# Optimization experiments

Measured on AMD Instinct MI355X. Metric: run time of the kernel, lower is better.

Reference implementation:

```python
import jax, jax.numpy as jnp
import numpy as np

B = 2_000_000
HID = 50
DIM = 2


def setup_inputs() -> dict:
    key = jax.random.key(0)
    k_y, k_w1, k_w2 = jax.random.split(key, 3)
    y = jax.random.normal(k_y, (B, DIM), dtype=jnp.float32)
    # weights ~ N(0, 0.1), biases = 0, matching the torch init
    W1 = 0.1 * jax.random.normal(k_w1, (HID, DIM), dtype=jnp.float32)
    b1 = jnp.zeros((HID,), dtype=jnp.float32)
    W2 = 0.1 * jax.random.normal(k_w2, (DIM, HID), dtype=jnp.float32)
    b2 = jnp.zeros((DIM,), dtype=jnp.float32)
    t = jnp.float32(0.0)
    return {"t": t, "y": y, "W1": W1, "b1": b1, "W2": W2, "b2": b2}


def reference(t, y, W1, b1, W2, b2):
    # Linear(2->50) + tanh + Linear(50->2); t is unused by the ODE func body.
    h = jnp.tanh(y @ W1.T + b1)  # [B, 50]
    return h @ W2.T + b2          # [B, 2]
```

## Files before the change

kernel.cpp:

```cpp
#include <hip/hip_runtime.h>


#define NROWS 2000000
#define HID 50
#define ROWS_PER_THREAD 4

__global__ __launch_bounds__(256) void odefunc_kernel(
    const float* __restrict__ y,
    const float* __restrict__ W1,
    const float* __restrict__ b1,
    const float* __restrict__ W2,
    const float* __restrict__ b2,
    float* __restrict__ out)
{
    const int tid = blockIdx.x * blockDim.x + threadIdx.x;
    const long long row0 = (long long)tid * ROWS_PER_THREAD;
    if (row0 >= NROWS) return;

    const float4 a = *reinterpret_cast<const float4*>(y + row0 * 2);
    const float4 b = *reinterpret_cast<const float4*>(y + row0 * 2 + 4);

    float y0[ROWS_PER_THREAD], y1[ROWS_PER_THREAD];
    y0[0] = a.x; y1[0] = a.y;
    y0[1] = a.z; y1[1] = a.w;
    y0[2] = b.x; y1[2] = b.y;
    y0[3] = b.z; y1[3] = b.w;

    const float bias0 = b2[0];
    const float bias1 = b2[1];

    float o0[ROWS_PER_THREAD], o1[ROWS_PER_THREAD];
#pragma unroll
    for (int r = 0; r < ROWS_PER_THREAD; ++r) { o0[r] = bias0; o1[r] = bias1; }

    const float TWO_LOG2E = 2.8853900817779268f;

#pragma unroll
    for (int j = 0; j < HID; ++j) {
        const float w0 = W1[2 * j];
        const float w1 = W1[2 * j + 1];
        const float bb = b1[j];
        const float v0 = W2[j];
        const float v1 = W2[HID + j];
#pragma unroll
        for (int r = 0; r < ROWS_PER_THREAD; ++r) {
            float z = fmaf(w0, y0[r], fmaf(w1, y1[r], bb));
            float e = __builtin_amdgcn_exp2f(z * TWO_LOG2E);
            float h = fmaf(-2.0f, __builtin_amdgcn_rcpf(e + 1.0f), 1.0f);
            o0[r] = fmaf(v0, h, o0[r]);
            o1[r] = fmaf(v1, h, o1[r]);
        }
    }

    float4 s0, s1;
    s0.x = o0[0]; s0.y = o1[0]; s0.z = o0[1]; s0.w = o1[1];
    s1.x = o0[2]; s1.y = o1[2]; s1.z = o0[3]; s1.w = o1[3];
    *reinterpret_cast<float4*>(out + row0 * 2) = s0;
    *reinterpret_cast<float4*>(out + row0 * 2 + 4) = s1;
}

extern "C" void kernel_launch(void* const* d_in, const int* in_sizes, int n_in,
                              void* d_out, int out_size, void* d_ws, size_t ws_size,
                              hipStream_t stream) {
    const float* y  = (const float*)d_in[1];
    const float* W1 = (const float*)d_in[2];
    const float* b1 = (const float*)d_in[3];
    const float* W2 = (const float*)d_in[4];
    const float* b2 = (const float*)d_in[5];
    float* out = (float*)d_out;

    const int threads_needed = NROWS / ROWS_PER_THREAD;
    const int block = 256;
    const int grid = (threads_needed + block - 1) / block;

    odefunc_kernel<<<grid, block, 0, stream>>>(y, W1, b1, W2, b2, out);
}
```

Before: 104.0 us.

## Fold tanh constants into preprocessed weights and process two rows per thread

A small prep kernel pre-scales W1 and b1 by 2*log2(e), pre-multiplies W2 by -2, and folds sum(W2)+b2 into the output bias. This removes the per-element multiply and FMA from the tanh evaluation in the main loop. The main kernel now handles 2 rows per thread instead of 4, giving twice as many threads. It reads the packed, zero-padded weights with vector loads in chunks of 8, which runs 56 hidden units where 50 are needed, and adds a second kernel launch.

New measurement: 104.9 us. About the same (+0.9%).

```diff
diff --git a/kernel.cpp b/kernel.cpp
--- a/kernel.cpp
+++ b/kernel.cpp
@@ -3,60 +3,75 @@
 
 #define NROWS 2000000
 #define HID 50
-#define ROWS_PER_THREAD 4
+#define C2L 2.8853900817779268f
 
-__global__ __launch_bounds__(256) void odefunc_kernel(
-    const float* __restrict__ y,
-    const float* __restrict__ W1,
-    const float* __restrict__ b1,
-    const float* __restrict__ W2,
-    const float* __restrict__ b2,
-    float* __restrict__ out)
-{
-    const int tid = blockIdx.x * blockDim.x + threadIdx.x;
-    const long long row0 = (long long)tid * ROWS_PER_THREAD;
-    if (row0 >= NROWS) return;
+__global__ void prep_kernel(const float* __restrict__ W1, const float* __restrict__ b1,
+                            const float* __restrict__ W2, const float* __restrict__ b2,
+                            float* __restrict__ w) {
+    const int j = threadIdx.x;
+    float wa = 0.f, wb = 0.f, wc = 0.f, va = 0.f, vb = 0.f;
+    float t0 = 0.f, t1 = 0.f;
+    if (j < HID) {
+        wa = W1[2 * j] * C2L;
+        wb = W1[2 * j + 1] * C2L;
+        wc = b1[j] * C2L;
+        t0 = W2[j];
+        t1 = W2[HID + j];
+        va = -2.0f * t0;
+        vb = -2.0f * t1;
+    }
+    w[j] = wa; w[64 + j] = wb; w[128 + j] = wc; w[192 + j] = va; w[256 + j] = vb;
+#pragma unroll
+    for (int off = 32; off > 0; off >>= 1) {
+        t0 += __shfl_down(t0, off, 64);
+        t1 += __shfl_down(t1, off, 64);
+    }
+    if (j == 0) { w[320] = b2[0] + t0; w[321] = b2[1] + t1; }
+}
 
-    const float4 a = *reinterpret_cast<const float4*>(y + row0 * 2);
-    const float4 b = *reinterpret_cast<const float4*>(y + row0 * 2 + 4);
+__global__ __launch_bounds__(256) void ode_main(const float* __restrict__ y,
+                                                const float* __restrict__ w,
+                                                float* __restrict__ out) {
+    const int tid = blockIdx.x * 256 + threadIdx.x;
+    if (tid >= NROWS / 2) return;
 
-    float y0[ROWS_PER_THREAD], y1[ROWS_PER_THREAD];
-    y0[0] = a.x; y1[0] = a.y;
-    y0[1] = a.z; y1[1] = a.w;
-    y0[2] = b.x; y1[2] = b.y;
-    y0[3] = b.z; y1[3] = b.w;
+    const float4 yv = reinterpret_cast<const float4*>(y)[tid];
+    const float y0a = yv.x, y0b = yv.y;
+    const float y1a = yv.z, y1b = yv.w;
 
-    const float bias0 = b2[0];
-    const float bias1 = b2[1];
-
-    float o0[ROWS_PER_THREAD], o1[ROWS_PER_THREAD];
-#pragma unroll
-    for (int r = 0; r < ROWS_PER_THREAD; ++r) { o0[r] = bias0; o1[r] = bias1; }
-
-    const float TWO_LOG2E = 2.8853900817779268f;
+    float o00 = w[320], o01 = w[321];
+    float o10 = o00,    o11 = o01;
 
 #pragma unroll
-    for (int j = 0; j < HID; ++j) {
-        const float w0 = W1[2 * j];
-        const float w1 = W1[2 * j + 1];
-        const float bb = b1[j];
-        const float v0 = W2[j];
-        const float v1 = W2[HID + j];
+    for (int c = 0; c < 56; c += 8) {
+        float wa[8], wb_[8], wc_[8], va[8], vb[8];
+        *(float4*)&wa[0]  = *(const float4*)(w + c);
+        *(float4*)&wa[4]  = *(const float4*)(w + c + 4);
+        *(float4*)&wb_[0] = *(const float4*)(w + 64 + c);
+        *(float4*)&wb_[4] = *(const float4*)(w + 64 + c + 4);
+        *(float4*)&wc_[0] = *(const float4*)(w + 128 + c);
+        *(float4*)&wc_[4] = *(const float4*)(w + 128 + c + 4);
+        *(float4*)&va[0]  = *(const float4*)(w + 192 + c);
+        *(float4*)&va[4]  = *(const float4*)(w + 192 + c + 4);
+        *(float4*)&vb[0]  = *(const float4*)(w + 256 + c);
+        *(float4*)&vb[4]  = *(const float4*)(w + 256 + c + 4);
 #pragma unroll
-        for (int r = 0; r < ROWS_PER_THREAD; ++r) {
-            float z = fmaf(w0, y0[r], fmaf(w1, y1[r], bb));
-            float e = __builtin_amdgcn_exp2f(z * TWO_LOG2E);
-            float h = fmaf(-2.0f, __builtin_amdgcn_rcpf(e + 1.0f), 1.0f);
-            o0[r] = fmaf(v0, h, o0[r]);
-            o1[r] = fmaf(v1, h, o1[r]);
+        for (int k = 0; k < 8; ++k) {
+            float z0 = fmaf(wa[k], y0a, fmaf(wb_[k], y0b, wc_[k]));
+            float z1 = fmaf(wa[k], y1a, fmaf(wb_[k], y1b, wc_[k]));
+            float e0 = __builtin_amdgcn_exp2f(z0);
+            float e1 = __builtin_amdgcn_exp2f(z1);
+            float r0 = __builtin_amdgcn_rcpf(e0 + 1.0f);
+            float r1 = __builtin_amdgcn_rcpf(e1 + 1.0f);
+            o00 = fmaf(va[k], r0, o00);
+            o01 = fmaf(vb[k], r0, o01);
+            o10 = fmaf(va[k], r1, o10);
+            o11 = fmaf(vb[k], r1, o11);
         }
     }
 
-    float4 s0, s1;
-    s0.x = o0[0]; s0.y = o1[0]; s0.z = o0[1]; s0.w = o1[1];
-    s1.x = o0[2]; s1.y = o1[2]; s1.z = o0[3]; s1.w = o1[3];
-    *reinterpret_cast<float4*>(out + row0 * 2) = s0;
-    *reinterpret_cast<float4*>(out + row0 * 2 + 4) = s1;
+    float4 s; s.x = o00; s.y = o01; s.z = o10; s.w = o11;
+    reinterpret_cast<float4*>(out)[tid] = s;
 }
 
 extern "C" void kernel_launch(void* const* d_in, const int* in_sizes, int n_in,
@@ -68,10 +83,11 @@
     const float* W2 = (const float*)d_in[4];
     const float* b2 = (const float*)d_in[5];
     float* out = (float*)d_out;
+    float* w   = (float*)d_ws;
 
-    const int threads_needed = NROWS / ROWS_PER_THREAD;
-    const int block = 256;
-    const int grid = (threads_needed + block - 1) / block;
+    prep_kernel<<<1, 64, 0, stream>>>(W1, b1, W2, b2, w);
 
-    odefunc_kernel<<<grid, block, 0, stream>>>(y, W1, b1, W2, b2, out);
+    const int threads = NROWS / 2;
+    const int grid = (threads + 255) / 256;
+    ode_main<<<grid, 256, 0, stream>>>(y, w, out);
 }
```
